# Performance work log

Measured on AMD Instinct MI355X. Metric: run time of the kernel, lower is better.

The kernel has to match this reference:

```python
import jax, jax.numpy as jnp
import numpy as np

EMB_DIM = 768
HEADS = 12
HEAD_DIM = EMB_DIM // HEADS  # 64


def setup_inputs() -> dict:
    key = jax.random.key(0)
    ks = jax.random.split(key, 9)
    s = 1.0 / np.sqrt(EMB_DIM)
    d = dict(
        x=jax.random.normal(ks[0], (2, 2048, EMB_DIM), dtype=jnp.float32),
        wq_w=jax.random.normal(ks[1], (EMB_DIM, EMB_DIM), dtype=jnp.float32) * s,
        wq_b=jax.random.normal(ks[2], (EMB_DIM,), dtype=jnp.float32) * 0.01,
        wk_w=jax.random.normal(ks[3], (EMB_DIM, EMB_DIM), dtype=jnp.float32) * s,
        wk_b=jax.random.normal(ks[4], (EMB_DIM,), dtype=jnp.float32) * 0.01,
        wv_w=jax.random.normal(ks[5], (EMB_DIM, EMB_DIM), dtype=jnp.float32) * s,
        wv_b=jax.random.normal(ks[6], (EMB_DIM,), dtype=jnp.float32) * 0.01,
        wo_w=jax.random.normal(ks[7], (EMB_DIM, EMB_DIM), dtype=jnp.float32) * s,
        wo_b=jax.random.normal(ks[8], (EMB_DIM,), dtype=jnp.float32) * 0.01,
    )
    return d


def reference(x, wq_w, wq_b, wk_w, wk_b, wv_w, wv_b, wo_w, wo_b):
    b, n, _ = x.shape
    # Linear projections (torch Linear: x @ W^T + b). q scaled by 1/8 == 1/sqrt(head_dim).
    q = (x @ wq_w.T + wq_b) / 8.0
    k = x @ wk_w.T + wk_b
    v = x @ wv_w.T + wv_b
    # [b, h, n, d]
    q = q.reshape(b, n, HEADS, HEAD_DIM).transpose(0, 2, 1, 3)
    k = k.reshape(b, n, HEADS, HEAD_DIM).transpose(0, 2, 1, 3)
    v = v.reshape(b, n, HEADS, HEAD_DIM).transpose(0, 2, 1, 3)
    # Full [b, h, n, n] score matrix with causal mask (strict upper triangle = -inf)
    scores = jnp.einsum('bhqd,bhkd->bhqk', q, k)
    causal = jnp.tril(jnp.ones((n, n), dtype=bool))  # True where allowed
    scores = jnp.where(causal[None, None], scores, -jnp.inf)
    attn = jax.nn.softmax(scores, axis=-1)
    out = jnp.einsum('bhqk,bhkd->bhqd', attn, v)
    out = out.transpose(0, 2, 1, 3).reshape(b, n, EMB_DIM)
    return out @ wo_w.T + wo_b
```

## Files before the change

### kernel.cpp

```cpp
#include <hip/hip_runtime.h>
#include <hip/hip_bf16.h>
#include <math.h>

#define EMB  768
#define NH   12
#define HD   64
#define SEQ  2048
#define BATCH 2
#define NTOK 4096

typedef __attribute__((ext_vector_type(8))) short short8;
typedef __attribute__((ext_vector_type(4))) float float4v;

static __device__ __forceinline__ short f2bf(float f) {
    __hip_bfloat16 h = __float2bfloat16(f);
    return *reinterpret_cast<short*>(&h);
}

static __device__ __forceinline__ void gll16(const void* g, void* l) {
    __builtin_amdgcn_global_load_lds(
        (const __attribute__((address_space(1))) void*)g,
        (__attribute__((address_space(3))) void*)l, 16, 0, 0);
}

__global__ __launch_bounds__(256) void cast_kernel(
    const float* __restrict__ x,  const float* __restrict__ wq,
    const float* __restrict__ wk, const float* __restrict__ wv,
    const float* __restrict__ wo,
    __hip_bfloat16* __restrict__ xb,  __hip_bfloat16* __restrict__ wqb,
    __hip_bfloat16* __restrict__ wkb, __hip_bfloat16* __restrict__ wvb,
    __hip_bfloat16* __restrict__ wob)
{
    const size_t S0 = (size_t)NTOK * EMB;
    const size_t S1 = (size_t)EMB * EMB;
    size_t i = ((size_t)blockIdx.x * 256 + threadIdx.x) * 8;
    const float* src; __hip_bfloat16* dst; size_t off;
    if      (i < S0)            { src = x;  dst = xb;  off = i; }
    else if (i < S0 + S1)       { src = wq; dst = wqb; off = i - S0; }
    else if (i < S0 + 2 * S1)   { src = wk; dst = wkb; off = i - S0 - S1; }
    else if (i < S0 + 3 * S1)   { src = wv; dst = wvb; off = i - S0 - 2 * S1; }
    else                        { src = wo; dst = wob; off = i - S0 - 3 * S1; }
    float4 f0 = *(const float4*)&src[off];
    float4 f1 = *(const float4*)&src[off + 4];
    short8 o;
    o[0] = f2bf(f0.x); o[1] = f2bf(f0.y); o[2] = f2bf(f0.z); o[3] = f2bf(f0.w);
    o[4] = f2bf(f1.x); o[5] = f2bf(f1.y); o[6] = f2bf(f1.z); o[7] = f2bf(f1.w);
    *(short8*)&dst[off] = o;
}

__global__ __launch_bounds__(256) void qkv_mfma_kernel(
    const __hip_bfloat16* __restrict__ xb,
    const __hip_bfloat16* __restrict__ wqb, const float* __restrict__ bq,
    const __hip_bfloat16* __restrict__ wkb, const float* __restrict__ bk,
    const __hip_bfloat16* __restrict__ wvb, const float* __restrict__ bv,
    __hip_bfloat16* __restrict__ q, __hip_bfloat16* __restrict__ k,
    __hip_bfloat16* __restrict__ vT)
{
    __shared__ __align__(16) short SM[16384];
    short* As = SM;
    short* Bs = SM + 8192;
    const int t = threadIdx.x;
    const int w = t >> 6, lane = t & 63;
    const int col = lane & 15, quad = lane >> 4;
    const int wm = w >> 1, wn = w & 1;
    const int m0 = blockIdx.y * 128;
    const int mat = blockIdx.x / 6;
    const int jj0 = (blockIdx.x % 6) * 128;
    const short* X = (const short*)xb;
    const short* W = (const short*)((mat == 0) ? wqb : (mat == 1) ? wkb : wvb);
    const float* bias = (mat == 0) ? bq : (mat == 1) ? bk : bv;

    float4v acc[4][4];
    #pragma unroll
    for (int mi = 0; mi < 4; ++mi)
        #pragma unroll
        for (int ni = 0; ni < 4; ++ni) acc[mi][ni] = (float4v){0.f, 0.f, 0.f, 0.f};

    for (int kb = 0; kb < EMB; kb += 64) {
        #pragma unroll
        for (int c = 0; c < 4; ++c) {
            int I = w * 256 + c * 64 + lane;
            int row = I >> 3;
            int c8 = (I & 7) ^ (row & 7);
            gll16(X + (size_t)(m0 + row) * EMB + kb + c8 * 8,
                  &As[(w * 256 + c * 64) * 8]);
            gll16(W + (size_t)(jj0 + row) * EMB + kb + c8 * 8,
                  &Bs[(w * 256 + c * 64) * 8]);
        }
        __syncthreads();
        #pragma unroll
        for (int ks = 0; ks < 2; ++ks) {
            short8 a[4], b[4];
            #pragma unroll
            for (int mi = 0; mi < 4; ++mi) {
                int row = wm * 64 + mi * 16 + col;
                a[mi] = *(short8*)&As[row * 64 + (((ks * 4 + quad) ^ (row & 7)) * 8)];
            }
            #pragma unroll
            for (int ni = 0; ni < 4; ++ni) {
                int row = wn * 64 + ni * 16 + col;
                b[ni] = *(short8*)&Bs[row * 64 + (((ks * 4 + quad) ^ (row & 7)) * 8)];
            }
            #pragma unroll
            for (int mi = 0; mi < 4; ++mi)
                #pragma unroll
                for (int ni = 0; ni < 4; ++ni)
                    acc[mi][ni] = __builtin_amdgcn_mfma_f32_16x16x32_bf16(
                        a[mi], b[ni], acc[mi][ni], 0, 0, 0);
        }
        __syncthreads();
    }
    const int bi = m0 >> 11, n0g = m0 & (SEQ - 1);
    if (mat != 2) {
        const float scale = (mat == 0) ? 0.125f * 1.44269504088896f : 1.0f;
        __hip_bfloat16* dstqk = (mat == 0) ? q : k;
        #pragma unroll
        for (int mi = 0; mi < 4; ++mi) {
            #pragma unroll
            for (int ni = 0; ni < 4; ++ni) {
                int gj = jj0 + wn * 64 + ni * 16 + col;
                int h = gj >> 6, d = gj & 63;
                float bsv = bias[gj];
                #pragma unroll
                for (int r = 0; r < 4; ++r) {
                    int gm = m0 + wm * 64 + mi * 16 + quad * 4 + r;
                    int bb = gm >> 11, n = gm & (SEQ - 1);
                    dstqk[(((size_t)bb * NH + h) * SEQ + n) * HD + d] =
                        __float2bfloat16((acc[mi][ni][r] + bsv) * scale);
                }
            }
        }
    } else {
        #pragma unroll
        for (int mi = 0; mi < 4; ++mi)
            #pragma unroll
            for (int ni = 0; ni < 4; ++ni) {
                int d_l = wn * 64 + ni * 16 + col;
                float bsv = bias[jj0 + d_l];
                #pragma unroll
                for (int r = 0; r < 4; ++r) {
                    int n_l = wm * 64 + mi * 16 + quad * 4 + r;
                    SM[(d_l << 7) + ((((n_l >> 3) ^ col) << 3) | (n_l & 7))] =
                        f2bf(acc[mi][ni][r] + bsv);
                }
            }
        __syncthreads();
        #pragma unroll
        for (int it = 0; it < 8; ++it) {
            int I = it * 256 + t;
            int d_l = I >> 4, c8 = I & 15;
            short8 val = *(short8*)&SM[(d_l << 7) + (c8 << 3)];
            int n_l = (c8 ^ (d_l & 15)) << 3;
            int gj = jj0 + d_l;
            int h = gj >> 6, dd = gj & 63;
            *(short8*)&vT[(((size_t)bi * NH + h) * HD + dd) * SEQ + n0g + n_l] = val;
        }
    }
}

__global__ __launch_bounds__(256) void attn_mfma_kernel(
    const __hip_bfloat16* __restrict__ qg, const __hip_bfloat16* __restrict__ kg,
    const __hip_bfloat16* __restrict__ vTg, __hip_bfloat16* __restrict__ ao,
    float* __restrict__ Os0, float* __restrict__ Os1,
    float* __restrict__ l0, float* __restrict__ l1)
{
    __shared__ __align__(16) short Ks[2][64 * 64];
    __shared__ __align__(16) short Vt[2][64 * 64];
    __shared__ __align__(16) short Ps[4][32][72];
    const int t = threadIdx.x;
    const int w = t >> 6, lane = t & 63;
    const int col = lane & 15, quad = lane >> 4;
    const int id = blockIdx.x;
    const int bh = id % 24;
    const int x = id / 24;
    int b, c;
    if (x < 8) { b = 8 + x; c = 0; }
    else {
        int i = x - 8, j = i >> 1;
        if ((i & 1) == 0) { b = 7 - j;  c = 0; }
        else              { b = 15 - j; c = 1; }
    }
    const int kt0 = c * 16;
    const int ktend = (kt0 + 16 < 2 * b + 2) ? kt0 + 16 : 2 * b + 2;
    const int niter = ktend - kt0;
    const bool single = (b <= 7);
    const int q0 = b * 128;
    const size_t base = (size_t)bh * SEQ * HD;
    const short* kp = (const short*)kg + base;
    const short* vp = (const short*)vTg + base;
    const short* qp = (const short*)qg + base;

    short8 qa[2][2];
    #pragma unroll
    for (int mi = 0; mi < 2; ++mi) {
        int qrow = q0 + (2 * w + mi) * 16 + col;
        #pragma unroll
        for (int ks = 0; ks < 2; ++ks)
            qa[mi][ks] = *(const short8*)&qp[(size_t)qrow * HD + ks * 32 + quad * 8];
    }
    float4v accO[2][4];
    float lacc[2][4];
    #pragma unroll
    for (int mi = 0; mi < 2; ++mi) {
        #pragma unroll
        for (int di = 0; di < 4; ++di) accO[mi][di] = (float4v){0.f, 0.f, 0.f, 0.f};
        #pragma unroll
        for (int r = 0; r < 4; ++r) lacc[mi][r] = 0.f;
    }

    {
        const int k0 = kt0 * 64;
        #pragma unroll
        for (int cc = 0; cc < 2; ++cc) {
            int I = w * 128 + cc * 64 + lane;
            int row = I >> 3;
            int c8 = (I & 7) ^ (row & 7);
            gll16(kp + (size_t)(k0 + row) * HD + c8 * 8, &Ks[0][(w * 128 + cc * 64) * 8]);
            gll16(vp + (size_t)row * SEQ + k0 + c8 * 8, &Vt[0][(w * 128 + cc * 64) * 8]);
        }
    }

    for (int lk = 0; lk < niter; ++lk) {
        const int kt = kt0 + lk;
        const int cur = lk & 1;
        const int k0 = kt * 64;
        __syncthreads();
        if (lk + 1 < niter) {
            const int kn = k0 + 64;
            #pragma unroll
            for (int cc = 0; cc < 2; ++cc) {
                int I = w * 128 + cc * 64 + lane;
                int row = I >> 3;
                int c8 = (I & 7) ^ (row & 7);
                gll16(kp + (size_t)(kn + row) * HD + c8 * 8,
                      &Ks[cur ^ 1][(w * 128 + cc * 64) * 8]);
                gll16(vp + (size_t)row * SEQ + kn + c8 * 8,
                      &Vt[cur ^ 1][(w * 128 + cc * 64) * 8]);
            }
        }
        const short* Kc = &Ks[cur][0];
        const short* Vc = &Vt[cur][0];

        float4v s[2][4];
        #pragma unroll
        for (int mi = 0; mi < 2; ++mi)
            #pragma unroll
            for (int ni = 0; ni < 4; ++ni) s[mi][ni] = (float4v){0.f, 0.f, 0.f, 0.f};
        #pragma unroll
        for (int ks = 0; ks < 2; ++ks)
            #pragma unroll
            for (int ni = 0; ni < 4; ++ni) {
                int row = ni * 16 + col;
                short8 kf = *(short8*)&Kc[row * 64 + (((ks * 4 + quad) ^ (row & 7)) * 8)];
                #pragma unroll
                for (int mi = 0; mi < 2; ++mi)
                    s[mi][ni] = __builtin_amdgcn_mfma_f32_16x16x32_bf16(
                        qa[mi][ks], kf, s[mi][ni], 0, 0, 0);
            }

        if (k0 >= q0) {
            #pragma unroll
            for (int mi = 0; mi < 2; ++mi)
                #pragma unroll
                for (int ni = 0; ni < 4; ++ni) {
                    int gcol = k0 + ni * 16 + col;
                    #pragma unroll
                    for (int r = 0; r < 4; ++r) {
                        int grow = q0 + (2 * w + mi) * 16 + quad * 4 + r;
                        s[mi][ni][r] = (gcol > grow) ? 0.f : exp2f(s[mi][ni][r]);
                    }
                }
        } else {
            #pragma unroll
            for (int mi = 0; mi < 2; ++mi)
                #pragma unroll
                for (int ni = 0; ni < 4; ++ni)
                    #pragma unroll
                    for (int r = 0; r < 4; ++r)
                        s[mi][ni][r] = exp2f(s[mi][ni][r]);
        }
        #pragma unroll
        for (int mi = 0; mi < 2; ++mi)
            #pragma unroll
            for (int r = 0; r < 4; ++r)
                lacc[mi][r] += (s[mi][0][r] + s[mi][1][r]) + (s[mi][2][r] + s[mi][3][r]);

        #pragma unroll
        for (int mi = 0; mi < 2; ++mi)
            #pragma unroll
            for (int ni = 0; ni < 4; ++ni)
                #pragma unroll
                for (int r = 0; r < 4; ++r)
                    Ps[w][mi * 16 + quad * 4 + r][ni * 16 + col] = f2bf(s[mi][ni][r]);
        short8 pa[2][2];
        #pragma unroll
        for (int mi = 0; mi < 2; ++mi)
            #pragma unroll
            for (int ks = 0; ks < 2; ++ks)
                pa[mi][ks] = *(short8*)&Ps[w][mi * 16 + col][ks * 32 + quad * 8];

        #pragma unroll
        for (int ks = 0; ks < 2; ++ks)
            #pragma unroll
            for (int di = 0; di < 4; ++di) {
                int row = di * 16 + col;
                short8 vf = *(short8*)&Vc[row * 64 + (((ks * 4 + quad) ^ (row & 7)) * 8)];
                #pragma unroll
                for (int mi = 0; mi < 2; ++mi)
                    accO[mi][di] = __builtin_amdgcn_mfma_f32_16x16x32_bf16(
                        pa[mi][ks], vf, accO[mi][di], 0, 0, 0);
            }
    }

    #pragma unroll
    for (int msk = 1; msk < 16; msk <<= 1)
        #pragma unroll
        for (int mi = 0; mi < 2; ++mi)
            #pragma unroll
            for (int r = 0; r < 4; ++r)
                lacc[mi][r] += __shfl_xor(lacc[mi][r], msk);

    const int bi = bh / NH, h = bh % NH;
    if (single) {
        #pragma unroll
        for (int mi = 0; mi < 2; ++mi)
            #pragma unroll
            for (int r = 0; r < 4; ++r) {
                float inv = 1.0f / lacc[mi][r];
                int n = q0 + (2 * w + mi) * 16 + quad * 4 + r;
                #pragma unroll
                for (int di = 0; di < 4; ++di)
                    ao[((size_t)bi * SEQ + n) * EMB + h * HD + di * 16 + col] =
                        __float2bfloat16(accO[mi][di][r] * inv);
            }
    } else {
        float* Os = c ? Os1 : Os0;
        float* ls = c ? l1 : l0;
        #pragma unroll
        for (int mi = 0; mi < 2; ++mi)
            #pragma unroll
            for (int r = 0; r < 4; ++r) {
                int n = q0 + (2 * w + mi) * 16 + quad * 4 + r;
                int nn = n - 1024;
                size_t rowb = ((size_t)bi * 1024 + nn) * EMB + h * HD;
                #pragma unroll
                for (int di = 0; di < 4; ++di)
                    Os[rowb + di * 16 + col] = accO[mi][di][r];
                if (col == 0)
                    ls[((size_t)bi * 1024 + nn) * NH + h] = lacc[mi][r];
            }
    }
}

__global__ __launch_bounds__(256) void combine_kernel(
    const float* __restrict__ Os0, const float* __restrict__ Os1,
    const float* __restrict__ l0, const float* __restrict__ l1,
    __hip_bfloat16* __restrict__ ao)
{
    size_t e8 = ((size_t)blockIdx.x * 256 + threadIdx.x) * 8;
    int u = e8 / EMB;
    int within = e8 % EMB;
    int h = within >> 6;
    int bi = u >> 10, nn = u & 1023;
    float inv = 1.0f / (l0[(size_t)u * NH + h] + l1[(size_t)u * NH + h]);
    float4 a0 = *(const float4*)&Os0[e8];
    float4 a1 = *(const float4*)&Os0[e8 + 4];
    float4 b0 = *(const float4*)&Os1[e8];
    float4 b1 = *(const float4*)&Os1[e8 + 4];
    short8 o;
    o[0] = f2bf((a0.x + b0.x) * inv); o[1] = f2bf((a0.y + b0.y) * inv);
    o[2] = f2bf((a0.z + b0.z) * inv); o[3] = f2bf((a0.w + b0.w) * inv);
    o[4] = f2bf((a1.x + b1.x) * inv); o[5] = f2bf((a1.y + b1.y) * inv);
    o[6] = f2bf((a1.z + b1.z) * inv); o[7] = f2bf((a1.w + b1.w) * inv);
    *(short8*)&ao[((size_t)bi * SEQ + 1024 + nn) * EMB + within] = o;
}

__global__ __launch_bounds__(256) void out_proj_mfma_kernel(
    const __hip_bfloat16* __restrict__ a, const __hip_bfloat16* __restrict__ wob,
    const float* __restrict__ bias, float* __restrict__ out)
{
    __shared__ __align__(16) short As[64 * 64];
    __shared__ __align__(16) short Bs[128 * 64];
    const int t = threadIdx.x;
    const int w = t >> 6, lane = t & 63;
    const int col = lane & 15, quad = lane >> 4;
    const int m0 = blockIdx.y * 64;
    const int n0 = blockIdx.x * 128;
    const short* A = (const short*)a;
    const short* W = (const short*)wob;

    float4v acc[4][2];
    #pragma unroll
    for (int mi = 0; mi < 4; ++mi)
        #pragma unroll
        for (int ni = 0; ni < 2; ++ni) acc[mi][ni] = (float4v){0.f, 0.f, 0.f, 0.f};

    for (int kb = 0; kb < EMB; kb += 64) {
        #pragma unroll
        for (int c = 0; c < 2; ++c) {
            int I = w * 128 + c * 64 + lane;
            int row = I >> 3;
            int c8 = (I & 7) ^ (row & 7);
            gll16(A + (size_t)(m0 + row) * EMB + kb + c8 * 8,
                  &As[(w * 128 + c * 64) * 8]);
        }
        #pragma unroll
        for (int c = 0; c < 4; ++c) {
            int I = w * 256 + c * 64 + lane;
            int row = I >> 3;
            int c8 = (I & 7) ^ (row & 7);
            gll16(W + (size_t)(n0 + row) * EMB + kb + c8 * 8,
                  &Bs[(w * 256 + c * 64) * 8]);
        }
        __syncthreads();
        #pragma unroll
        for (int ks = 0; ks < 2; ++ks) {
            short8 av[4], bv[2];
            #pragma unroll
            for (int mi = 0; mi < 4; ++mi) {
                int row = mi * 16 + col;
                av[mi] = *(short8*)&As[row * 64 + (((ks * 4 + quad) ^ (row & 7)) * 8)];
            }
            #pragma unroll
            for (int ni = 0; ni < 2; ++ni) {
                int row = w * 32 + ni * 16 + col;
                bv[ni] = *(short8*)&Bs[row * 64 + (((ks * 4 + quad) ^ (row & 7)) * 8)];
            }
            #pragma unroll
            for (int mi = 0; mi < 4; ++mi)
                #pragma unroll
                for (int ni = 0; ni < 2; ++ni)
                    acc[mi][ni] = __builtin_amdgcn_mfma_f32_16x16x32_bf16(
                        av[mi], bv[ni], acc[mi][ni], 0, 0, 0);
        }
        __syncthreads();
    }
    #pragma unroll
    for (int mi = 0; mi < 4; ++mi)
        #pragma unroll
        for (int ni = 0; ni < 2; ++ni) {
            int gj = n0 + w * 32 + ni * 16 + col;
            float bsv = bias[gj];
            #pragma unroll
            for (int r = 0; r < 4; ++r) {
                int gm = m0 + mi * 16 + quad * 4 + r;
                out[(size_t)gm * EMB + gj] = acc[mi][ni][r] + bsv;
            }
        }
}

extern "C" void kernel_launch(void* const* d_in, const int* in_sizes, int n_in,
                              void* d_out, int out_size, void* d_ws, size_t ws_size,
                              hipStream_t stream) {
    const float* x  = (const float*)d_in[0];
    const float* wq = (const float*)d_in[1];
    const float* bq = (const float*)d_in[2];
    const float* wk = (const float*)d_in[3];
    const float* bk = (const float*)d_in[4];
    const float* wv = (const float*)d_in[5];
    const float* bv = (const float*)d_in[6];
    const float* wo = (const float*)d_in[7];
    const float* bo = (const float*)d_in[8];
    float* out = (float*)d_out;

    const size_t TOK = (size_t)NTOK * EMB;
    const size_t WSZ = (size_t)EMB * EMB;
    __hip_bfloat16* xb  = (__hip_bfloat16*)d_ws;
    __hip_bfloat16* wqb = xb  + TOK;
    __hip_bfloat16* wkb = wqb + WSZ;
    __hip_bfloat16* wvb = wkb + WSZ;
    __hip_bfloat16* wob = wvb + WSZ;
    __hip_bfloat16* qb  = wob + WSZ;
    __hip_bfloat16* kb  = qb  + TOK;
    __hip_bfloat16* vTb = kb  + TOK;
    __hip_bfloat16* aob = vTb + TOK;
    float* Os0 = (float*)d_ws;
    float* Os1 = (float*)(aob + TOK);
    float* l0  = Os1 + (size_t)2 * 1024 * EMB;
    float* l1  = l0  + (size_t)2 * 1024 * NH;

    cast_kernel<<<2688, 256, 0, stream>>>(x, wq, wk, wv, wo, xb, wqb, wkb, wvb, wob);
    qkv_mfma_kernel<<<dim3(18, 32), 256, 0, stream>>>(xb, wqb, bq, wkb, bk, wvb, bv,
                                                      qb, kb, vTb);
    attn_mfma_kernel<<<576, 256, 0, stream>>>(qb, kb, vTb, aob, Os0, Os1, l0, l1);
    combine_kernel<<<768, 256, 0, stream>>>(Os0, Os1, l0, l1, aob);
    out_proj_mfma_kernel<<<dim3(6, 64), 256, 0, stream>>>(aob, wob, bo, out);
}
```

Baseline: 172.2 us.

## Load K/V fragments directly from global into registers, dropping LDS staging

The attention kernel no longer stages K and V tiles through double-buffered shared memory with async global-to-LDS loads and per-iteration barriers. Each wave now loads its MFMA K and V operand fragments straight from global memory into registers. A launch-bounds occupancy hint of 2 is also added. This removes LDS traffic and __syncthreads, but all four waves now fetch the same K/V data redundantly from global/L2, and the loads are no longer prefetched ahead of use, which risks exposed memory latency.

```diff
diff --git a/kernel.cpp b/kernel.cpp
--- a/kernel.cpp
+++ b/kernel.cpp
@@ -158,14 +158,12 @@
     }
 }
 
-__global__ __launch_bounds__(256) void attn_mfma_kernel(
+__global__ __launch_bounds__(256, 2) void attn_mfma_kernel(
     const __hip_bfloat16* __restrict__ qg, const __hip_bfloat16* __restrict__ kg,
     const __hip_bfloat16* __restrict__ vTg, __hip_bfloat16* __restrict__ ao,
     float* __restrict__ Os0, float* __restrict__ Os1,
     float* __restrict__ l0, float* __restrict__ l1)
 {
-    __shared__ __align__(16) short Ks[2][64 * 64];
-    __shared__ __align__(16) short Vt[2][64 * 64];
     __shared__ __align__(16) short Ps[4][32][72];
     const int t = threadIdx.x;
     const int w = t >> 6, lane = t & 63;
@@ -208,38 +206,25 @@
         for (int r = 0; r < 4; ++r) lacc[mi][r] = 0.f;
     }
 
-    {
-        const int k0 = kt0 * 64;
-        #pragma unroll
-        for (int cc = 0; cc < 2; ++cc) {
-            int I = w * 128 + cc * 64 + lane;
-            int row = I >> 3;
-            int c8 = (I & 7) ^ (row & 7);
-            gll16(kp + (size_t)(k0 + row) * HD + c8 * 8, &Ks[0][(w * 128 + cc * 64) * 8]);
-            gll16(vp + (size_t)row * SEQ + k0 + c8 * 8, &Vt[0][(w * 128 + cc * 64) * 8]);
-        }
-    }
+    const short* kbase = kp + (size_t)col * HD + quad * 8;
+    const short* vbase = vp + (size_t)col * SEQ + quad * 8;
 
     for (int lk = 0; lk < niter; ++lk) {
         const int kt = kt0 + lk;
-        const int cur = lk & 1;
         const int k0 = kt * 64;
-        __syncthreads();
-        if (lk + 1 < niter) {
-            const int kn = k0 + 64;
-            #pragma unroll
-            for (int cc = 0; cc < 2; ++cc) {
-                int I = w * 128 + cc * 64 + lane;
-                int row = I >> 3;
-                int c8 = (I & 7) ^ (row & 7);
-                gll16(kp + (size_t)(kn + row) * HD + c8 * 8,
-                      &Ks[cur ^ 1][(w * 128 + cc * 64) * 8]);
-                gll16(vp + (size_t)row * SEQ + kn + c8 * 8,
-                      &Vt[cur ^ 1][(w * 128 + cc * 64) * 8]);
-            }
-        }
-        const short* Kc = &Ks[cur][0];
-        const short* Vc = &Vt[cur][0];
+
+        short8 kf[2][4];
+        #pragma unroll
+        for (int ks = 0; ks < 2; ++ks)
+            #pragma unroll
+            for (int ni = 0; ni < 4; ++ni)
+                kf[ks][ni] = *(const short8*)(kbase + (size_t)(k0 + ni * 16) * HD + ks * 32);
+        short8 vf[2][4];
+        #pragma unroll
+        for (int ks = 0; ks < 2; ++ks)
+            #pragma unroll
+            for (int di = 0; di < 4; ++di)
+                vf[ks][di] = *(const short8*)(vbase + (size_t)(di * 16) * SEQ + k0 + ks * 32);
 
         float4v s[2][4];
         #pragma unroll
@@ -249,14 +234,11 @@
         #pragma unroll
         for (int ks = 0; ks < 2; ++ks)
             #pragma unroll
-            for (int ni = 0; ni < 4; ++ni) {
-                int row = ni * 16 + col;
-                short8 kf = *(short8*)&Kc[row * 64 + (((ks * 4 + quad) ^ (row & 7)) * 8)];
+            for (int ni = 0; ni < 4; ++ni)
                 #pragma unroll
                 for (int mi = 0; mi < 2; ++mi)
                     s[mi][ni] = __builtin_amdgcn_mfma_f32_16x16x32_bf16(
-                        qa[mi][ks], kf, s[mi][ni], 0, 0, 0);
-            }
+                        qa[mi][ks], kf[ks][ni], s[mi][ni], 0, 0, 0);
 
         if (k0 >= q0) {
             #pragma unroll
@@ -302,14 +284,11 @@
         #pragma unroll
         for (int ks = 0; ks < 2; ++ks)
             #pragma unroll
-            for (int di = 0; di < 4; ++di) {
-                int row = di * 16 + col;
-                short8 vf = *(short8*)&Vc[row * 64 + (((ks * 4 + quad) ^ (row & 7)) * 8)];
+            for (int di = 0; di < 4; ++di)
                 #pragma unroll
                 for (int mi = 0; mi < 2; ++mi)
                     accO[mi][di] = __builtin_amdgcn_mfma_f32_16x16x32_bf16(
-                        pa[mi][ks], vf, accO[mi][di], 0, 0, 0);
-            }
+                        pa[mi][ks], vf[ks][di], accO[mi][di], 0, 0, 0);
     }
 
     #pragma unroll
```

Result: slower. 192.3 us (+11.7%).
